# Performance work log

Hardware: AMD Instinct MI355X
Metric: run time of the kernel (lower is better)

## Reference

```python
import jax, jax.numpy as jnp
import numpy as np


def setup_inputs() -> dict:
    key = jax.random.key(0)
    ks = jax.random.split(key, 8)
    B, C, D, H, W = 2, 32, 16, 16, 16
    C8 = C // 8
    x = jax.random.normal(ks[0], (B, C, D, H, W), dtype=jnp.float32)
    s = 1.0 / np.sqrt(C)
    wq = jax.random.normal(ks[1], (C8, C), dtype=jnp.float32) * s
    bq = jnp.zeros((C8,), dtype=jnp.float32)
    wk = jax.random.normal(ks[2], (C8, C), dtype=jnp.float32) * s
    bk = jnp.zeros((C8,), dtype=jnp.float32)
    wv = jax.random.normal(ks[3], (C, C), dtype=jnp.float32) * s
    bv = jnp.zeros((C,), dtype=jnp.float32)
    gamma_p = jnp.ones((1,), dtype=jnp.float32)
    gamma_c = jnp.ones((1,), dtype=jnp.float32)
    wo = jax.random.normal(ks[4], (C, 2 * C), dtype=jnp.float32) * (1.0 / np.sqrt(2 * C))
    bo = jnp.zeros((C,), dtype=jnp.float32)
    return {"x": x, "wq": wq, "bq": bq, "wk": wk, "bk": bk,
            "wv": wv, "bv": bv, "gamma_p": gamma_p, "gamma_c": gamma_c,
            "wo": wo, "bo": bo}


def _forward(x, wq, bq, wk, bk, wv, bv, gamma_p, gamma_c, wo, bo):
    B, C, D, H, W = x.shape
    N = D * H * W
    xf = x.reshape(B, C, N)  # [B, C, N]

    # ---- PAM: position attention over N = D*H*W tokens ----
    # 1x1x1 Conv3d == per-token channel matmul
    q = jnp.einsum('oc,bcn->bno', wq, xf) + bq            # [B, N, C/8]
    k = jnp.einsum('oc,bcn->bon', wk, xf) + bk[None, :, None]  # [B, C/8, N]
    v = jnp.einsum('oc,bcn->bon', wv, xf) + bv[None, :, None]  # [B, C, N]
    energy = jnp.einsum('bno,bom->bnm', q, k)             # [B, N, N] (unscaled)
    attn = jax.nn.softmax(energy, axis=-1)                # rows over keys
    # out = v @ attn^T : out[b,c,i] = sum_j v[b,c,j] * attn[b,i,j]
    pam_out = jnp.einsum('bcj,bij->bci', v, attn)         # [B, C, N]
    pam = (gamma_p[0] * pam_out + xf).reshape(B, C, D, H, W)

    # ---- CAM: channel attention with max-subtraction softmax ----
    eng = jnp.einsum('bcn,bdn->bcd', xf, xf)              # [B, C, C]
    eng_new = jnp.max(eng, axis=-1, keepdims=True) - eng
    cattn = jax.nn.softmax(eng_new, axis=-1)              # [B, C, C]
    cam_out = jnp.einsum('bcd,bdn->bcn', cattn, xf)       # [B, C, N]
    cam = (gamma_c[0] * cam_out + xf).reshape(B, C, D, H, W)

    # ---- concat + 1x1x1 out conv ----
    cat = jnp.concatenate([pam, cam], axis=1).reshape(B, 2 * C, N)
    out = jnp.einsum('oc,bcn->bon', wo, cat) + bo[None, :, None]
    return out.reshape(B, C, D, H, W)


def reference(x, wq, bq, wk, bk, wv, bv, gamma_p, gamma_c, wo, bo):
    return _forward(x, wq, bq, wk, bk, wv, bv, gamma_p, gamma_c, wo, bo)
```

## Files before the change

### kernel.cpp

```cpp
#include <hip/hip_runtime.h>
#include <hip/hip_bf16.h>
#include <math.h>

#define BB 2
#define CC 32
#define C8 4
#define NN 4096
#define VST 72
#define LOG2E 1.4426950408889634f

typedef __attribute__((ext_vector_type(8))) short short8;
typedef __attribute__((ext_vector_type(16))) float f32x16;

static __device__ __forceinline__ short f2bf(float x) {
    return __builtin_bit_cast(short, __float2bfloat16(x));
}
static __device__ __forceinline__ unsigned int pkbf(float a, float b) {
    unsigned int ua = __builtin_bit_cast(unsigned int, a) + 0x8000u;
    unsigned int ub = __builtin_bit_cast(unsigned int, b) + 0x8000u;
    return (ua >> 16) | (ub & 0xffff0000u);
}

__global__ __launch_bounds__(256) void k1(const float* __restrict__ x,
    const float* __restrict__ wq, const float* __restrict__ bq,
    const float* __restrict__ wk, const float* __restrict__ bk,
    const float* __restrict__ wv, const float* __restrict__ bv,
    short* __restrict__ qpk, short* __restrict__ kpk, short* __restrict__ vbf,
    float* __restrict__ eng)
{
    if (blockIdx.x >= 32) {
        int w = threadIdx.x >> 6, lane = threadIdx.x & 63;
        int pp = (blockIdx.x - 32)*4 + w;
        int b = pp >= 528 ? 1 : 0;
        int t = pp - b*528;
        int c = 0, rem = t;
        while (rem >= CC - c) { rem -= CC - c; ++c; }
        int d = c + rem;
        const float4* xc = (const float4*)(x + ((size_t)b*CC + c)*NN);
        const float4* xd = (const float4*)(x + ((size_t)b*CC + d)*NN);
        float s = 0.f;
        for (int tt = lane; tt < NN/4; tt += 64) {
            float4 a = xc[tt], bb = xd[tt];
            s += a.x*bb.x + a.y*bb.y + a.z*bb.z + a.w*bb.w;
        }
        #pragma unroll
        for (int off = 32; off; off >>= 1) s += __shfl_down(s, off, 64);
        if (lane == 0) {
            eng[(b*CC + c)*CC + d] = s;
            eng[(b*CC + d)*CC + c] = s;
        }
        return;
    }
    __shared__ float swq[C8*CC], swk[C8*CC], swv[CC*CC], sbq[C8], sbk[C8], sbv[CC];
    int tid = threadIdx.x;
    for (int i = tid; i < C8*CC; i += 256) { swq[i] = wq[i]; swk[i] = wk[i]; }
    for (int i = tid; i < CC*CC; i += 256) swv[i] = wv[i];
    if (tid < C8) { sbq[tid] = bq[tid]; sbk[tid] = bk[tid]; }
    if (tid < CC) sbv[tid] = bv[tid];
    __syncthreads();
    int g = blockIdx.x*256 + tid;
    int b = g >> 12; int n = g & (NN-1);
    const float* xb = x + (size_t)b*CC*NN + n;
    float xr[CC];
    #pragma unroll
    for (int c = 0; c < CC; ++c) xr[c] = xb[(size_t)c*NN];
    float qv[C8], kv[C8];
    #pragma unroll
    for (int o = 0; o < C8; ++o) { qv[o] = sbq[o]; kv[o] = sbk[o]; }
    #pragma unroll
    for (int c = 0; c < CC; ++c) {
        float xc = xr[c];
        #pragma unroll
        for (int o = 0; o < C8; ++o) { qv[o] += swq[o*CC+c]*xc; kv[o] += swk[o*CC+c]*xc; }
    }
    short4 qs = make_short4(f2bf(qv[0]*LOG2E), f2bf(qv[1]*LOG2E),
                            f2bf(qv[2]*LOG2E), f2bf(qv[3]*LOG2E));
    short4 ks = make_short4(f2bf(kv[0]), f2bf(kv[1]), f2bf(kv[2]), f2bf(kv[3]));
    *(short4*)(qpk + ((size_t)b*NN + n)*4) = qs;
    *(short4*)(kpk + ((size_t)b*NN + n)*4) = ks;
    #pragma unroll
    for (int o = 0; o < CC; ++o) {
        float av = sbv[o];
        #pragma unroll
        for (int c = 0; c < CC; ++c) av += swv[o*CC+c]*xr[c];
        vbf[((size_t)b*CC+o)*NN + n] = f2bf(av);
    }
}

__global__ __launch_bounds__(512, 2) void k2(const short* __restrict__ qpk,
    const short* __restrict__ kpk, const short* __restrict__ vbf,
    const float* __restrict__ eng, const float* __restrict__ wo,
    const float* __restrict__ bo, const float* __restrict__ gp,
    const float* __restrict__ gc, const float* __restrict__ x,
    float* __restrict__ out)
{
    __shared__ __align__(16) char smem[73728];

    int blk = blockIdx.x;
    int b  = blk >> 7;
    int it = blk & 127;
    int i0 = it*32;
    int tid = threadIdx.x;
    int w = tid >> 6, lane = tid & 63;
    int qcol = lane & 31, h = lane >> 5;

    short* vb0 = (short*)smem + w*2*(32*VST);
    short* vb1 = vb0 + 32*VST;

    int rv = lane >> 1, ch = lane & 1;
    const short* vsrc = vbf + (size_t)b*CC*NN + (size_t)rv*NN + w*64 + ch*32;
    const short* ksrc = kpk + ((size_t)b*NN + w*64 + qcol)*4;

    short8 qf = {0,0,0,0,0,0,0,0};
    if (h == 0) {
        short4 qv = *(const short4*)(qpk + ((size_t)b*NN + i0 + qcol)*4);
        qf[0]=qv.x; qf[1]=qv.y; qf[2]=qv.z; qf[3]=qv.w;
    }

    f32x16 acc = {0,0,0,0,0,0,0,0,0,0,0,0,0,0,0,0};
    const f32x16 zz = {0,0,0,0,0,0,0,0,0,0,0,0,0,0,0,0};
    float se = 0.f;

    short8 cv0 = *(const short8*)(vsrc);
    short8 cv1 = *(const short8*)(vsrc + 8);
    short8 cv2 = *(const short8*)(vsrc + 16);
    short8 cv3 = *(const short8*)(vsrc + 24);
    short4 ck0 = *(const short4*)(ksrc);
    short4 ck1 = *(const short4*)(ksrc + 128);

    #pragma unroll
    for (int t = 0; t < 8; ++t) {
        int tn = t < 7 ? t + 1 : 7;
        short8 nv0 = *(const short8*)(vsrc + tn*512);
        short8 nv1 = *(const short8*)(vsrc + tn*512 + 8);
        short8 nv2 = *(const short8*)(vsrc + tn*512 + 16);
        short8 nv3 = *(const short8*)(vsrc + tn*512 + 24);
        short4 nk0 = *(const short4*)(ksrc + tn*2048);
        short4 nk1 = *(const short4*)(ksrc + tn*2048 + 128);

        short* wb = (t & 1) ? vb1 : vb0;
        short* wp = wb + rv*VST + ch*32;
        *(short8*)(wp)      = cv0;
        *(short8*)(wp + 8)  = cv1;
        *(short8*)(wp + 16) = cv2;
        *(short8*)(wp + 24) = cv3;

        const short* vrow = wb + qcol*VST;
        #pragma unroll
        for (int cI = 0; cI < 2; ++cI) {
            short4 kk = cI ? ck1 : ck0;
            short8 kf = {kk.x, kk.y, kk.z, kk.w, 0,0,0,0};
            f32x16 s = __builtin_amdgcn_mfma_f32_32x32x16_bf16(kf, qf, zz, 0, 0, 0);
            float p[16];
            #pragma unroll
            for (int i = 0; i < 16; ++i) p[i] = exp2f(s[i]);
            se += (((p[0]+p[1])+(p[2]+p[3])) + ((p[4]+p[5])+(p[6]+p[7])))
                + (((p[8]+p[9])+(p[10]+p[11])) + ((p[12]+p[13])+(p[14]+p[15])));
            unsigned int u0 = pkbf(p[0],p[1]),   u1 = pkbf(p[2],p[3]);
            unsigned int u2 = pkbf(p[4],p[5]),   u3 = pkbf(p[6],p[7]);
            unsigned int u4 = pkbf(p[8],p[9]),   u5 = pkbf(p[10],p[11]);
            unsigned int u6 = pkbf(p[12],p[13]), u7 = pkbf(p[14],p[15]);
            int vo = cI*32 + 4*h;
            short4 a0 = *(const short4*)(vrow + vo);
            short4 a1 = *(const short4*)(vrow + vo + 8);
            short4 a2 = *(const short4*)(vrow + vo + 16);
            short4 a3 = *(const short4*)(vrow + vo + 24);
            short8 vf1 = {a0.x,a0.y,a0.z,a0.w, a1.x,a1.y,a1.z,a1.w};
            short8 pf1 = {(short)u0,(short)(u0>>16),(short)u1,(short)(u1>>16),
                          (short)u2,(short)(u2>>16),(short)u3,(short)(u3>>16)};
            acc = __builtin_amdgcn_mfma_f32_32x32x16_bf16(vf1, pf1, acc, 0, 0, 0);
            short8 vf2 = {a2.x,a2.y,a2.z,a2.w, a3.x,a3.y,a3.z,a3.w};
            short8 pf2 = {(short)u4,(short)(u4>>16),(short)u5,(short)(u5>>16),
                          (short)u6,(short)(u6>>16),(short)u7,(short)(u7>>16)};
            acc = __builtin_amdgcn_mfma_f32_32x32x16_bf16(vf2, pf2, acc, 0, 0, 0);
        }
        cv0 = nv0; cv1 = nv1; cv2 = nv2; cv3 = nv3;
        ck0 = nk0; ck1 = nk1;
    }

    se += __shfl_xor(se, 32, 64);

    __syncthreads();
    float* pamw = (float*)smem;
    float* seL  = pamw + 8448;
    float* sinv = seL  + 256;
    float* pamn = sinv + 32;
    float* xt   = pamn + 1056;
    float* swo  = xt   + 1056;
    float* swx  = swo  + 1056;
    float* sc   = swx  + 1056;
    float* seng = sc   + 1056;
    float* sbo  = seng + 1024;
    float* swo2 = sbo  + 32;

    #pragma unroll
    for (int r = 0; r < 16; ++r) {
        int c = (r&3) + 8*(r>>2) + 4*h;
        pamw[w*1056 + c*33 + qcol] = acc[r];
    }
    if (h == 0) seL[w*32 + qcol] = se;
    for (int i = tid; i < CC*CC; i += 512) {
        int o = i >> 5, c2 = i & 31;
        seng[i] = eng[b*CC*CC + i];
        swo [o*33 + c2] = wo[o*64 + c2];
        swo2[o*33 + c2] = wo[o*64 + 32 + c2];
        xt  [o*33 + c2] = x[(size_t)b*CC*NN + (size_t)o*NN + i0 + c2];
    }
    if (tid < CC) sbo[tid] = bo[tid];
    __syncthreads();

    if (tid < CC) {
        float s = 0.f;
        #pragma unroll
        for (int w2 = 0; w2 < 8; ++w2) s += seL[w2*32 + tid];
        sinv[tid] = 1.f / s;
    } else if (tid >= 64 && tid < 64 + CC) {
        int r2 = tid - 64;
        float mn = seng[r2*32];
        #pragma unroll
        for (int d = 1; d < CC; ++d) mn = fminf(mn, seng[r2*32 + d]);
        float pv[CC]; float s = 0.f;
        #pragma unroll
        for (int d = 0; d < CC; ++d) { pv[d] = __expf(mn - seng[r2*32 + d]); s += pv[d]; }
        float inv = 1.f / s;
        #pragma unroll
        for (int d = 0; d < CC; ++d) sc[r2*33 + d] = pv[d]*inv;
    }
    __syncthreads();

    float gpv = gp[0], gcv = gc[0];
    for (int i = tid; i < CC*CC; i += 512) {
        int c = i >> 5, q = i & 31;
        float s2 = 0.f;
        #pragma unroll
        for (int w2 = 0; w2 < 8; ++w2) s2 += pamw[w2*1056 + c*33 + q];
        pamn[c*33 + q] = gpv * s2 * sinv[q];
        float t2 = 0.f;
        #pragma unroll
        for (int c2 = 0; c2 < CC; ++c2) t2 += swo2[c*33 + c2] * sc[c2*33 + q];
        swx[c*33 + q] = swo[c*33 + q] + swo2[c*33 + q] + gcv * t2;
    }
    __syncthreads();

    int q = tid & 31, slot = tid >> 5;
    float o0 = sbo[slot], o1 = sbo[slot + 16];
    #pragma unroll
    for (int c = 0; c < CC; ++c) {
        float p  = pamn[c*33 + q];
        float xv = xt[c*33 + q];
        o0 += swo[slot*33 + c]      * p + swx[slot*33 + c]      * xv;
        o1 += swo[(slot+16)*33 + c] * p + swx[(slot+16)*33 + c] * xv;
    }
    float* ob = out + (size_t)b*CC*NN + i0 + q;
    ob[(size_t)slot*NN]      = o0;
    ob[(size_t)(slot+16)*NN] = o1;
}

extern "C" void kernel_launch(void* const* d_in, const int* in_sizes, int n_in,
                              void* d_out, int out_size, void* d_ws, size_t ws_size,
                              hipStream_t stream)
{
    const float* x  = (const float*)d_in[0];
    const float* wq = (const float*)d_in[1];
    const float* bq = (const float*)d_in[2];
    const float* wk = (const float*)d_in[3];
    const float* bk = (const float*)d_in[4];
    const float* wv = (const float*)d_in[5];
    const float* bv = (const float*)d_in[6];
    const float* gp = (const float*)d_in[7];
    const float* gc = (const float*)d_in[8];
    const float* wo = (const float*)d_in[9];
    const float* bo = (const float*)d_in[10];

    char* wsb = (char*)d_ws;
    short* qpk = (short*)(wsb + 0);
    short* kpk = (short*)(wsb + 65536);
    short* vbf = (short*)(wsb + 131072);
    float* eng = (float*)(wsb + 655360);

    k1<<<296, 256, 0, stream>>>(x, wq, bq, wk, bk, wv, bv, qpk, kpk, vbf, eng);
    k2<<<BB*128, 512, 0, stream>>>(qpk, kpk, vbf, eng, wo, bo, gp, gc, x, (float*)d_out);
}
```

Baseline: 30.35 us.

## Double threads per block in attention kernel and split V projection across halves

The projection kernel now handles 128 tokens per block. Each half of the block computes 16 of the 32 V output channels, and only the first half computes Q and K. The attention kernel grows to 1024 threads: 16 waves each cover a quarter of the key range, and the per-wave double buffer for V becomes a single buffer. The reductions and the epilogue are adjusted so each thread writes one output channel. The aim is more waves in flight for latency hiding. The risk is that the launch bound of (1024, 4) limits registers per thread and may cause spills, and that losing the double buffer exposes load latency.

```diff
diff --git a/kernel.cpp b/kernel.cpp
--- a/kernel.cpp
+++ b/kernel.cpp
@@ -28,9 +28,9 @@
     short* __restrict__ qpk, short* __restrict__ kpk, short* __restrict__ vbf,
     float* __restrict__ eng)
 {
-    if (blockIdx.x >= 32) {
+    if (blockIdx.x >= 64) {
         int w = threadIdx.x >> 6, lane = threadIdx.x & 63;
-        int pp = (blockIdx.x - 32)*4 + w;
+        int pp = (blockIdx.x - 64)*4 + w;
         int b = pp >= 528 ? 1 : 0;
         int t = pp - b*528;
         int c = 0, rem = t;
@@ -58,43 +58,47 @@
     if (tid < C8) { sbq[tid] = bq[tid]; sbk[tid] = bk[tid]; }
     if (tid < CC) sbv[tid] = bv[tid];
     __syncthreads();
-    int g = blockIdx.x*256 + tid;
+    int tl = tid & 127, oh = tid >> 7;
+    int g = blockIdx.x*128 + tl;
     int b = g >> 12; int n = g & (NN-1);
     const float* xb = x + (size_t)b*CC*NN + n;
     float xr[CC];
     #pragma unroll
     for (int c = 0; c < CC; ++c) xr[c] = xb[(size_t)c*NN];
-    float qv[C8], kv[C8];
-    #pragma unroll
-    for (int o = 0; o < C8; ++o) { qv[o] = sbq[o]; kv[o] = sbk[o]; }
-    #pragma unroll
-    for (int c = 0; c < CC; ++c) {
-        float xc = xr[c];
-        #pragma unroll
-        for (int o = 0; o < C8; ++o) { qv[o] += swq[o*CC+c]*xc; kv[o] += swk[o*CC+c]*xc; }
-    }
-    short4 qs = make_short4(f2bf(qv[0]*LOG2E), f2bf(qv[1]*LOG2E),
-                            f2bf(qv[2]*LOG2E), f2bf(qv[3]*LOG2E));
-    short4 ks = make_short4(f2bf(kv[0]), f2bf(kv[1]), f2bf(kv[2]), f2bf(kv[3]));
-    *(short4*)(qpk + ((size_t)b*NN + n)*4) = qs;
-    *(short4*)(kpk + ((size_t)b*NN + n)*4) = ks;
-    #pragma unroll
-    for (int o = 0; o < CC; ++o) {
-        float av = sbv[o];
-        #pragma unroll
-        for (int c = 0; c < CC; ++c) av += swv[o*CC+c]*xr[c];
-        vbf[((size_t)b*CC+o)*NN + n] = f2bf(av);
-    }
-}
-
-__global__ __launch_bounds__(512, 2) void k2(const short* __restrict__ qpk,
+    if (oh == 0) {
+        float qv[C8], kv[C8];
+        #pragma unroll
+        for (int o = 0; o < C8; ++o) { qv[o] = sbq[o]; kv[o] = sbk[o]; }
+        #pragma unroll
+        for (int c = 0; c < CC; ++c) {
+            float xc = xr[c];
+            #pragma unroll
+            for (int o = 0; o < C8; ++o) { qv[o] += swq[o*CC+c]*xc; kv[o] += swk[o*CC+c]*xc; }
+        }
+        short4 qs = make_short4(f2bf(qv[0]*LOG2E), f2bf(qv[1]*LOG2E),
+                                f2bf(qv[2]*LOG2E), f2bf(qv[3]*LOG2E));
+        short4 ks = make_short4(f2bf(kv[0]), f2bf(kv[1]), f2bf(kv[2]), f2bf(kv[3]));
+        *(short4*)(qpk + ((size_t)b*NN + n)*4) = qs;
+        *(short4*)(kpk + ((size_t)b*NN + n)*4) = ks;
+    }
+    int o0 = oh*16;
+    #pragma unroll
+    for (int o = 0; o < 16; ++o) {
+        float av = sbv[o0+o];
+        #pragma unroll
+        for (int c = 0; c < CC; ++c) av += swv[(o0+o)*CC+c]*xr[c];
+        vbf[((size_t)b*CC+o0+o)*NN + n] = f2bf(av);
+    }
+}
+
+__global__ __launch_bounds__(1024, 4) void k2(const short* __restrict__ qpk,
     const short* __restrict__ kpk, const short* __restrict__ vbf,
     const float* __restrict__ eng, const float* __restrict__ wo,
     const float* __restrict__ bo, const float* __restrict__ gp,
     const float* __restrict__ gc, const float* __restrict__ x,
     float* __restrict__ out)
 {
-    __shared__ __align__(16) char smem[73728];
+    __shared__ __align__(16) char smem[99328];
 
     int blk = blockIdx.x;
     int b  = blk >> 7;
@@ -104,8 +108,7 @@
     int w = tid >> 6, lane = tid & 63;
     int qcol = lane & 31, h = lane >> 5;
 
-    short* vb0 = (short*)smem + w*2*(32*VST);
-    short* vb1 = vb0 + 32*VST;
+    short* vbuf = (short*)smem + w*(32*VST);
 
     int rv = lane >> 1, ch = lane & 1;
     const short* vsrc = vbf + (size_t)b*CC*NN + (size_t)rv*NN + w*64 + ch*32;
@@ -129,23 +132,22 @@
     short4 ck1 = *(const short4*)(ksrc + 128);
 
     #pragma unroll
-    for (int t = 0; t < 8; ++t) {
-        int tn = t < 7 ? t + 1 : 7;
-        short8 nv0 = *(const short8*)(vsrc + tn*512);
-        short8 nv1 = *(const short8*)(vsrc + tn*512 + 8);
-        short8 nv2 = *(const short8*)(vsrc + tn*512 + 16);
-        short8 nv3 = *(const short8*)(vsrc + tn*512 + 24);
-        short4 nk0 = *(const short4*)(ksrc + tn*2048);
-        short4 nk1 = *(const short4*)(ksrc + tn*2048 + 128);
-
-        short* wb = (t & 1) ? vb1 : vb0;
-        short* wp = wb + rv*VST + ch*32;
+    for (int t = 0; t < 4; ++t) {
+        int tn = t < 3 ? t + 1 : 3;
+        short8 nv0 = *(const short8*)(vsrc + tn*1024);
+        short8 nv1 = *(const short8*)(vsrc + tn*1024 + 8);
+        short8 nv2 = *(const short8*)(vsrc + tn*1024 + 16);
+        short8 nv3 = *(const short8*)(vsrc + tn*1024 + 24);
+        short4 nk0 = *(const short4*)(ksrc + tn*4096);
+        short4 nk1 = *(const short4*)(ksrc + tn*4096 + 128);
+
+        short* wp = vbuf + rv*VST + ch*32;
         *(short8*)(wp)      = cv0;
         *(short8*)(wp + 8)  = cv1;
         *(short8*)(wp + 16) = cv2;
         *(short8*)(wp + 24) = cv3;
 
-        const short* vrow = wb + qcol*VST;
+        const short* vrow = vbuf + qcol*VST;
         #pragma unroll
         for (int cI = 0; cI < 2; ++cI) {
             short4 kk = cI ? ck1 : ck0;
@@ -182,8 +184,8 @@
 
     __syncthreads();
     float* pamw = (float*)smem;
-    float* seL  = pamw + 8448;
-    float* sinv = seL  + 256;
+    float* seL  = pamw + 16*1056;
+    float* sinv = seL  + 512;
     float* pamn = sinv + 32;
     float* xt   = pamn + 1056;
     float* swo  = xt   + 1056;
@@ -199,7 +201,7 @@
         pamw[w*1056 + c*33 + qcol] = acc[r];
     }
     if (h == 0) seL[w*32 + qcol] = se;
-    for (int i = tid; i < CC*CC; i += 512) {
+    for (int i = tid; i < CC*CC; i += 1024) {
         int o = i >> 5, c2 = i & 31;
         seng[i] = eng[b*CC*CC + i];
         swo [o*33 + c2] = wo[o*64 + c2];
@@ -212,7 +214,7 @@
     if (tid < CC) {
         float s = 0.f;
         #pragma unroll
-        for (int w2 = 0; w2 < 8; ++w2) s += seL[w2*32 + tid];
+        for (int w2 = 0; w2 < 16; ++w2) s += seL[w2*32 + tid];
         sinv[tid] = 1.f / s;
     } else if (tid >= 64 && tid < 64 + CC) {
         int r2 = tid - 64;
@@ -229,11 +231,11 @@
     __syncthreads();
 
     float gpv = gp[0], gcv = gc[0];
-    for (int i = tid; i < CC*CC; i += 512) {
+    for (int i = tid; i < CC*CC; i += 1024) {
         int c = i >> 5, q = i & 31;
         float s2 = 0.f;
         #pragma unroll
-        for (int w2 = 0; w2 < 8; ++w2) s2 += pamw[w2*1056 + c*33 + q];
+        for (int w2 = 0; w2 < 16; ++w2) s2 += pamw[w2*1056 + c*33 + q];
         pamn[c*33 + q] = gpv * s2 * sinv[q];
         float t2 = 0.f;
         #pragma unroll
@@ -242,18 +244,13 @@
     }
     __syncthreads();
 
-    int q = tid & 31, slot = tid >> 5;
-    float o0 = sbo[slot], o1 = sbo[slot + 16];
+    int q = tid & 31, slot = (tid >> 5) & 31;
+    float o0 = sbo[slot];
     #pragma unroll
     for (int c = 0; c < CC; ++c) {
-        float p  = pamn[c*33 + q];
-        float xv = xt[c*33 + q];
-        o0 += swo[slot*33 + c]      * p + swx[slot*33 + c]      * xv;
-        o1 += swo[(slot+16)*33 + c] * p + swx[(slot+16)*33 + c] * xv;
-    }
-    float* ob = out + (size_t)b*CC*NN + i0 + q;
-    ob[(size_t)slot*NN]      = o0;
-    ob[(size_t)(slot+16)*NN] = o1;
+        o0 += swo[slot*33 + c] * pamn[c*33 + q] + swx[slot*33 + c] * xt[c*33 + q];
+    }
+    out[(size_t)b*CC*NN + (size_t)slot*NN + i0 + q] = o0;
 }
 
 extern "C" void kernel_launch(void* const* d_in, const int* in_sizes, int n_in,
@@ -278,6 +275,6 @@
     short* vbf = (short*)(wsb + 131072);
     float* eng = (float*)(wsb + 655360);
 
-    k1<<<296, 256, 0, stream>>>(x, wq, bq, wk, bk, wv, bv, qpk, kpk, vbf, eng);
-    k2<<<BB*128, 512, 0, stream>>>(qpk, kpk, vbf, eng, wo, bo, gp, gc, x, (float*)d_out);
-}
+    k1<<<328, 256, 0, stream>>>(x, wq, bq, wk, bk, wv, bv, qpk, kpk, vbf, eng);
+    k2<<<BB*128, 1024, 0, stream>>>(qpk, kpk, vbf, eng, wo, bo, gp, gc, x, (float*)d_out);
+}
```

New measurement: 28.41 us. -6.4%, faster.
